# Performance work log

Hardware: AMD Instinct MI355X
Metric: run time of the kernel (lower is better)

The kernel has to match this reference:

```python
import jax, jax.numpy as jnp
import numpy as np

B, S, D, E, K = 2, 4096, 1024, 8, 2

def setup_inputs() -> dict:
    key = jax.random.key(0)
    k1, k2, k3, k4, k5 = jax.random.split(key, 5)
    x = jax.random.normal(k1, (B, S, D), dtype=jnp.float32)
    expert_weights = jax.random.uniform(k2, (B, S, K), dtype=jnp.float32)
    top_k_indices = jax.random.randint(k3, (B, S, K), 0, E, dtype=jnp.int32)
    W = jax.random.normal(k4, (E, D, D), dtype=jnp.float32) * (1.0 / np.sqrt(D))
    b = jax.random.normal(k5, (E, D), dtype=jnp.float32) * 0.01
    return {"x": x, "expert_weights": expert_weights,
            "top_k_indices": top_k_indices, "W": W, "b": b}

def reference(x, expert_weights, top_k_indices, W, b):
    # Dense all-expert linear: [B,S,E,Dout]
    expert_outputs = jnp.einsum('bsd,edf->bsef', x, W) + b  # bias broadcasts over b,s
    # Gather the top-k expert outputs per token: [B,S,K,Dout]
    gathered = jnp.take_along_axis(expert_outputs, top_k_indices[:, :, :, None], axis=2)
    # Weighted combine over k
    output = jnp.sum(expert_weights[:, :, :, None] * gathered, axis=2)
    return output
```

## Files before the change

kernel.cpp:

```cpp
#include <hip/hip_runtime.h>
#include <hip/hip_bf16.h>
#include <cstdio>
#include <cstdint>

static constexpr int TOK = 8192;
static constexpr int DIM = 1024;
static constexpr int NEXP = 8;
static constexpr int NGRP = 16;

typedef unsigned short u16;
typedef unsigned int u32;

using floatx4 = __attribute__((ext_vector_type(4))) float;
using bf16x8  = __attribute__((ext_vector_type(8))) __bf16;


__device__ __forceinline__ u16 f2bf(float f) {
  union { float f; u32 u; } v; v.f = f;
  u32 r = v.u + 0x7fffu + ((v.u >> 16) & 1u);
  return (u16)(r >> 16);
}

__device__ __forceinline__ float bf2f(u16 b) {
  union { u32 u; float f; } v; v.u = (u32)b << 16;
  return v.f;
}

__device__ __forceinline__ void gload_lds16(const void* g, void* l) {
  __builtin_amdgcn_global_load_lds(
      (const __attribute__((address_space(1))) void*)g,
      (__attribute__((address_space(3))) void*)l,
      16, 0, 0);
}

__global__ __launch_bounds__(1024)
void prep_kernel(const int* __restrict__ idx, const float* __restrict__ ew,
                 int* __restrict__ meta, int* __restrict__ tileMap,
                 int* __restrict__ tokList, float* __restrict__ wList,
                 int* __restrict__ posOf) {
  __shared__ int cnt2[16][NGRP];
  __shared__ int cur2[16][NGRP];
  __shared__ int tot[NGRP], offS[NGRP], tbase[NGRP];
  const int tid = threadIdx.x;
  const int wid = tid >> 6;
  if (tid < 16 * NGRP) ((int*)cnt2)[tid] = 0;
  __syncthreads();
  int gl[16];
#pragma unroll
  for (int j = 0; j < 16; ++j) {
    int i = tid + 1024 * j;
    int g = ((i & 1) << 3) | idx[i];
    gl[j] = g;
    atomicAdd(&cnt2[wid][g], 1);
  }
  __syncthreads();
  if (tid < NGRP) {
    int s = 0;
    for (int w = 0; w < 16; ++w) { cur2[w][tid] = s; s += cnt2[w][tid]; }
    tot[tid] = s;
  }
  __syncthreads();
  if (tid == 0) {
    int run = 0, t = 0, tk0 = 0;
    for (int g = 0; g < NGRP; ++g) {
      offS[g] = run; tbase[g] = t;
      t += (tot[g] + 127) >> 7;
      if (g == NEXP - 1) tk0 = t;
      run += tot[g];
    }
    meta[48] = t;
    meta[49] = tk0;
  }
  __syncthreads();
  if (tid < NGRP) {
    meta[tid] = tot[tid];
    meta[16 + tid] = offS[tid];
    int b = tbase[tid], n = (tot[tid] + 127) >> 7;
    for (int m0 = 0; m0 < n; ++m0) tileMap[b + m0] = (tid << 12) | m0;
  }
  if (tid < 16 * NGRP) {
    int w = tid >> 4, g = tid & 15;
    cur2[w][g] += offS[g];
  }
  __syncthreads();
#pragma unroll
  for (int j = 0; j < 16; ++j) {
    int i = tid + 1024 * j;
    int pos = atomicAdd(&cur2[wid][gl[j]], 1);
    tokList[pos] = i >> 1;
    wList[pos] = ew[i];
    posOf[i] = pos;
  }
}

__global__ __launch_bounds__(256)
void setup_kernel(const float* __restrict__ x, const int* __restrict__ posOf,
                  u16* __restrict__ Abuf, const float* __restrict__ W,
                  u16* __restrict__ wt) {
  const int bid = blockIdx.x;
  const int tid = threadIdx.x;
  if (bid < TOK) {
    const int t = bid;
    float4 v = reinterpret_cast<const float4*>(x + ((size_t)t << 10))[tid];
    ushort4 o;
    o.x = f2bf(v.x); o.y = f2bf(v.y); o.z = f2bf(v.z); o.w = f2bf(v.w);
    const int p0 = posOf[2 * t], p1 = posOf[2 * t + 1];
    reinterpret_cast<ushort4*>(Abuf + ((size_t)p0 << 10))[tid] = o;
    reinterpret_cast<ushort4*>(Abuf + ((size_t)p1 << 10))[tid] = o;
  } else {
    __shared__ u16 tile[32][33];
    const int b = bid - TOK;
    const int e = b >> 10;
    const int f0 = ((b >> 5) & 31) * 32, d0 = (b & 31) * 32;
    const float* src = W + ((size_t)e << 20);
    u16* dst = wt + ((size_t)e << 20);
    const int tx = tid & 31, ty = tid >> 5;
#pragma unroll
    for (int j = 0; j < 4; ++j) {
      int d = d0 + ty + 8 * j;
      tile[ty + 8 * j][tx] = f2bf(src[(size_t)d * DIM + f0 + tx]);
    }
    __syncthreads();
#pragma unroll
    for (int j = 0; j < 4; ++j) {
      int f = f0 + ty + 8 * j;
      dst[(size_t)f * DIM + d0 + tx] = tile[tx][ty + 8 * j];
    }
  }
}

__global__ __launch_bounds__(256, 4)
void moe_gemm_kernel(const u16* __restrict__ Abuf, const u16* __restrict__ wt,
                     const float* __restrict__ bias, const int* __restrict__ tokList,
                     const float* __restrict__ wList, const int* __restrict__ meta,
                     const int* __restrict__ tileMap, float* __restrict__ out,
                     u16* __restrict__ cbufA, u16* __restrict__ cbufB, int mode,
                     int pass) {
  constexpr int BM = 128, BN = 128, BK = 64;
  const int chunk = gridDim.y;
  int lin = blockIdx.y * 8 + blockIdx.x;
  int swz = (lin & 7) * chunk + (lin >> 3);
  int tileIdx = swz >> 3, nt = swz & 7;

  int tBase = 0, tEnd = meta[48];
  const int tilesK0 = meta[49];
  if (mode == 0) { if (pass == 0) tEnd = tilesK0; else tBase = tilesK0; }
  tileIdx += tBase;
  if (tileIdx >= tEnd) return;

  const int tm = tileMap[tileIdx];
  const int g = tm >> 12, m0 = tm & 0xfff;
  const int e = g & (NEXP - 1);
  const int nrem = meta[g] - m0 * BM;
  const int listBase = meta[16 + g] + m0 * BM;

  __shared__ __align__(16) u16 As[BM * BK];
  __shared__ __align__(16) u16 Bs[BN * BK];

  const int tid = threadIdx.x;
  const int rowA = tid >> 3;
  const int chnk = tid & 7;
  const int csw  = chnk ^ (rowA & 7);
  const u16* wb = wt + ((size_t)e << 20);
  const u16* ab = Abuf + ((size_t)listBase << 10);

  const int wid = tid >> 6, lane = tid & 63;
  const int wm = (wid >> 1) * 64, wn = (wid & 1) * 64;
  const int lr = lane & 15, lg = lane >> 4;
  const int rx = lr & 7;

  floatx4 acc[4][4];
#pragma unroll
  for (int i = 0; i < 4; ++i)
#pragma unroll
    for (int j = 0; j < 4; ++j) acc[i][j] = (floatx4){0.f, 0.f, 0.f, 0.f};

  for (int kt = 0; kt < DIM / BK; ++kt) {
    __syncthreads();
#pragma unroll
    for (int r = 0; r < 4; ++r) {
      const int row = rowA + 32 * r;
      gload_lds16(ab + ((size_t)row << 10) + kt * BK + csw * 8,
                  &As[row * BK + chnk * 8]);
    }
#pragma unroll
    for (int r = 0; r < 4; ++r) {
      const int row = rowA + 32 * r;
      gload_lds16(wb + ((size_t)(nt * BN + row) << 10) + kt * BK + csw * 8,
                  &Bs[row * BK + chnk * 8]);
    }
    asm volatile("s_waitcnt vmcnt(0)" ::: "memory");
    __syncthreads();

#pragma unroll
    for (int ks = 0; ks < 2; ++ks) {
      bf16x8 av[4], bv[4];
#pragma unroll
      for (int mi = 0; mi < 4; ++mi)
        av[mi] = *reinterpret_cast<const bf16x8*>(
            &As[(wm + mi * 16 + lr) * BK + (((ks * 4 + lg) ^ rx)) * 8]);
#pragma unroll
      for (int ni = 0; ni < 4; ++ni)
        bv[ni] = *reinterpret_cast<const bf16x8*>(
            &Bs[(wn + ni * 16 + lr) * BK + (((ks * 4 + lg) ^ rx)) * 8]);
#pragma unroll
      for (int mi = 0; mi < 4; ++mi)
#pragma unroll
        for (int ni = 0; ni < 4; ++ni)
          acc[mi][ni] = __builtin_amdgcn_mfma_f32_16x16x32_bf16(av[mi], bv[ni], acc[mi][ni], 0, 0, 0);
    }
  }

  u16* cb = nullptr;
  bool rmw = false, f32out = false;
  if (mode == 2)      cb = (g < NEXP) ? cbufA : cbufB;
  else if (mode == 1) { if (g < NEXP) f32out = true; else cb = cbufA; }
  else                { f32out = true; rmw = (pass == 1); }
  const float* bp = bias + e * DIM;
#pragma unroll
  for (int mi = 0; mi < 4; ++mi) {
#pragma unroll
    for (int r = 0; r < 4; ++r) {
      const int rl = wm + mi * 16 + lg * 4 + r;
      if (rl < nrem) {
        const int   tok = tokList[listBase + rl];
        const float w   = wList[listBase + rl];
        const size_t rowOff = (size_t)tok << 10;
#pragma unroll
        for (int ni = 0; ni < 4; ++ni) {
          const int col = nt * BN + wn + ni * 16 + lr;
          const float v = w * (acc[mi][ni][r] + bp[col]);
          if (f32out) { if (rmw) out[rowOff + col] += v; else out[rowOff + col] = v; }
          else        cb[rowOff + col] = f2bf(v);
        }
      }
    }
  }
}

__global__ __launch_bounds__(256)
void combine2_kernel(float* __restrict__ out, const u16* __restrict__ cbufA,
                     const u16* __restrict__ cbufB) {
  const int p = blockIdx.x * 256 + threadIdx.x;
  uint4 ca = reinterpret_cast<const uint4*>(cbufA)[p];
  uint4 cb = reinterpret_cast<const uint4*>(cbufB)[p];
  float4 r0, r1;
  r0.x = bf2f((u16)(ca.x & 0xffff)) + bf2f((u16)(cb.x & 0xffff));
  r0.y = bf2f((u16)(ca.x >> 16))    + bf2f((u16)(cb.x >> 16));
  r0.z = bf2f((u16)(ca.y & 0xffff)) + bf2f((u16)(cb.y & 0xffff));
  r0.w = bf2f((u16)(ca.y >> 16))    + bf2f((u16)(cb.y >> 16));
  r1.x = bf2f((u16)(ca.z & 0xffff)) + bf2f((u16)(cb.z & 0xffff));
  r1.y = bf2f((u16)(ca.z >> 16))    + bf2f((u16)(cb.z >> 16));
  r1.z = bf2f((u16)(ca.w & 0xffff)) + bf2f((u16)(cb.w & 0xffff));
  r1.w = bf2f((u16)(ca.w >> 16))    + bf2f((u16)(cb.w >> 16));
  float4* o4 = reinterpret_cast<float4*>(out) + 2 * (size_t)p;
  o4[0] = r0; o4[1] = r1;
}

__global__ __launch_bounds__(256)
void combine_kernel(float* __restrict__ out, const u16* __restrict__ cbuf) {
  const int p = blockIdx.x * 256 + threadIdx.x;
  uint4 c = reinterpret_cast<const uint4*>(cbuf)[p];
  float4* o4 = reinterpret_cast<float4*>(out) + 2 * (size_t)p;
  float4 a = o4[0], b = o4[1];
  a.x += bf2f((u16)(c.x & 0xffff)); a.y += bf2f((u16)(c.x >> 16));
  a.z += bf2f((u16)(c.y & 0xffff)); a.w += bf2f((u16)(c.y >> 16));
  b.x += bf2f((u16)(c.z & 0xffff)); b.y += bf2f((u16)(c.z >> 16));
  b.z += bf2f((u16)(c.w & 0xffff)); b.w += bf2f((u16)(c.w >> 16));
  o4[0] = a; o4[1] = b;
}

extern "C" void kernel_launch(void* const* d_in, const int* in_sizes, int n_in,
                              void* d_out, int out_size, void* d_ws, size_t ws_size,
                              hipStream_t stream) {
  const float* x    = (const float*)d_in[0];
  const float* ew   = (const float*)d_in[1];
  const int*   idx  = (const int*)d_in[2];
  const float* W    = (const float*)d_in[3];
  const float* bias = (const float*)d_in[4];
  float* out = (float*)d_out;

  char* ws = (char*)d_ws;
  u16*   Abuf  = (u16*)ws;
  u16*   wtp   = (u16*)(ws + ((size_t)32 << 20));
  u16*   cbufA = (u16*)(ws + ((size_t)48 << 20));
  u16*   cbufB = (u16*)(ws + ((size_t)64 << 20));

  const size_t tailSz = (size_t)(194 << 10);
  const size_t need0 = ((size_t)48 << 20) + tailSz;
  const size_t need1 = ((size_t)64 << 20) + tailSz;
  const size_t need2 = ((size_t)80 << 20) + tailSz;
  if (ws_size < need0) {
    fprintf(stderr, "kernel_launch: ws_size %zu < needed %zu\n", ws_size, need0);
    return;
  }
  const int mode = (ws_size >= need2) ? 2 : (ws_size >= need1) ? 1 : 0;
  char* tail = ws + ((mode == 2) ? ((size_t)80 << 20)
                                 : (mode == 1) ? ((size_t)64 << 20)
                                               : ((size_t)48 << 20));
  int*   tokList = (int*)tail;
  float* wList   = (float*)(tail + (64 << 10));
  int*   posOf   = (int*)(tail + (128 << 10));
  int*   meta    = (int*)(tail + (192 << 10));
  int*   tileMap = (int*)(tail + (193 << 10));

  prep_kernel<<<1, 1024, 0, stream>>>(idx, ew, meta, tileMap, tokList, wList, posOf);
  setup_kernel<<<TOK + 8192, 256, 0, stream>>>(x, posOf, Abuf, W, wtp);

  if (mode == 2) {
    moe_gemm_kernel<<<dim3(8, 144), 256, 0, stream>>>(
        Abuf, wtp, bias, tokList, wList, meta, tileMap, out, cbufA, cbufB, 2, 0);
    combine2_kernel<<<TOK * DIM / 8 / 256, 256, 0, stream>>>(out, cbufA, cbufB);
  } else if (mode == 1) {
    moe_gemm_kernel<<<dim3(8, 144), 256, 0, stream>>>(
        Abuf, wtp, bias, tokList, wList, meta, tileMap, out, cbufA, nullptr, 1, 0);
    combine_kernel<<<TOK * DIM / 8 / 256, 256, 0, stream>>>(out, cbufA);
  } else {
    moe_gemm_kernel<<<dim3(8, 72), 256, 0, stream>>>(
        Abuf, wtp, bias, tokList, wList, meta, tileMap, out, nullptr, nullptr, 0, 0);
    moe_gemm_kernel<<<dim3(8, 72), 256, 0, stream>>>(
        Abuf, wtp, bias, tokList, wList, meta, tileMap, out, nullptr, nullptr, 0, 1);
  }
}
```

Baseline: 116.5 us.

## Overlap routing prep with weight transpose and split x gather kernel

The single-block routing prep kernel now runs as an extra block inside the weight transpose/bf16 conversion launch, so it overlaps the weight work instead of running serially before it. The x gather/convert, which depends on posOf, moves into its own kernel launched afterwards. This takes the serial prep latency off the critical path. In exchange there is one extra launch, and the prep block now uses 256 threads doing 64 iterations each, so it runs longer on a single CU and could become the tail of the combined kernel.

```diff
diff --git a/kernel.cpp b/kernel.cpp
--- a/kernel.cpp
+++ b/kernel.cpp
@@ -33,85 +33,18 @@
       16, 0, 0);
 }
 
-__global__ __launch_bounds__(1024)
-void prep_kernel(const int* __restrict__ idx, const float* __restrict__ ew,
-                 int* __restrict__ meta, int* __restrict__ tileMap,
-                 int* __restrict__ tokList, float* __restrict__ wList,
-                 int* __restrict__ posOf) {
-  __shared__ int cnt2[16][NGRP];
-  __shared__ int cur2[16][NGRP];
-  __shared__ int tot[NGRP], offS[NGRP], tbase[NGRP];
-  const int tid = threadIdx.x;
-  const int wid = tid >> 6;
-  if (tid < 16 * NGRP) ((int*)cnt2)[tid] = 0;
-  __syncthreads();
-  int gl[16];
-#pragma unroll
-  for (int j = 0; j < 16; ++j) {
-    int i = tid + 1024 * j;
-    int g = ((i & 1) << 3) | idx[i];
-    gl[j] = g;
-    atomicAdd(&cnt2[wid][g], 1);
-  }
-  __syncthreads();
-  if (tid < NGRP) {
-    int s = 0;
-    for (int w = 0; w < 16; ++w) { cur2[w][tid] = s; s += cnt2[w][tid]; }
-    tot[tid] = s;
-  }
-  __syncthreads();
-  if (tid == 0) {
-    int run = 0, t = 0, tk0 = 0;
-    for (int g = 0; g < NGRP; ++g) {
-      offS[g] = run; tbase[g] = t;
-      t += (tot[g] + 127) >> 7;
-      if (g == NEXP - 1) tk0 = t;
-      run += tot[g];
-    }
-    meta[48] = t;
-    meta[49] = tk0;
-  }
-  __syncthreads();
-  if (tid < NGRP) {
-    meta[tid] = tot[tid];
-    meta[16 + tid] = offS[tid];
-    int b = tbase[tid], n = (tot[tid] + 127) >> 7;
-    for (int m0 = 0; m0 < n; ++m0) tileMap[b + m0] = (tid << 12) | m0;
-  }
-  if (tid < 16 * NGRP) {
-    int w = tid >> 4, g = tid & 15;
-    cur2[w][g] += offS[g];
-  }
-  __syncthreads();
-#pragma unroll
-  for (int j = 0; j < 16; ++j) {
-    int i = tid + 1024 * j;
-    int pos = atomicAdd(&cur2[wid][gl[j]], 1);
-    tokList[pos] = i >> 1;
-    wList[pos] = ew[i];
-    posOf[i] = pos;
-  }
-}
-
 __global__ __launch_bounds__(256)
-void setup_kernel(const float* __restrict__ x, const int* __restrict__ posOf,
-                  u16* __restrict__ Abuf, const float* __restrict__ W,
-                  u16* __restrict__ wt) {
+void trans_prep_kernel(const float* __restrict__ W, u16* __restrict__ wt,
+                       const int* __restrict__ idx, const float* __restrict__ ew,
+                       int* __restrict__ meta, int* __restrict__ tileMap,
+                       int* __restrict__ tokList, float* __restrict__ wList,
+                       int* __restrict__ posOf) {
   const int bid = blockIdx.x;
   const int tid = threadIdx.x;
-  if (bid < TOK) {
-    const int t = bid;
-    float4 v = reinterpret_cast<const float4*>(x + ((size_t)t << 10))[tid];
-    ushort4 o;
-    o.x = f2bf(v.x); o.y = f2bf(v.y); o.z = f2bf(v.z); o.w = f2bf(v.w);
-    const int p0 = posOf[2 * t], p1 = posOf[2 * t + 1];
-    reinterpret_cast<ushort4*>(Abuf + ((size_t)p0 << 10))[tid] = o;
-    reinterpret_cast<ushort4*>(Abuf + ((size_t)p1 << 10))[tid] = o;
-  } else {
+  if (bid < 8192) {
     __shared__ u16 tile[32][33];
-    const int b = bid - TOK;
-    const int e = b >> 10;
-    const int f0 = ((b >> 5) & 31) * 32, d0 = (b & 31) * 32;
+    const int e = bid >> 10;
+    const int f0 = ((bid >> 5) & 31) * 32, d0 = (bid & 31) * 32;
     const float* src = W + ((size_t)e << 20);
     u16* dst = wt + ((size_t)e << 20);
     const int tx = tid & 31, ty = tid >> 5;
@@ -126,7 +59,69 @@
       int f = f0 + ty + 8 * j;
       dst[(size_t)f * DIM + d0 + tx] = tile[tx][ty + 8 * j];
     }
-  }
+  } else {
+    __shared__ int cnt2[4][NGRP];
+    __shared__ int cur2[4][NGRP];
+    __shared__ int tot[NGRP], offS[NGRP], tbase[NGRP];
+    const int wid = tid >> 6;
+    if (tid < 4 * NGRP) ((int*)cnt2)[tid] = 0;
+    __syncthreads();
+    for (int j = 0; j < 64; ++j) {
+      int i = tid + 256 * j;
+      int g = ((i & 1) << 3) | idx[i];
+      atomicAdd(&cnt2[wid][g], 1);
+    }
+    __syncthreads();
+    if (tid < NGRP) {
+      int s = 0;
+      for (int w = 0; w < 4; ++w) { cur2[w][tid] = s; s += cnt2[w][tid]; }
+      tot[tid] = s;
+    }
+    __syncthreads();
+    if (tid == 0) {
+      int run = 0, t = 0, tk0 = 0;
+      for (int g = 0; g < NGRP; ++g) {
+        offS[g] = run; tbase[g] = t;
+        t += (tot[g] + 127) >> 7;
+        if (g == NEXP - 1) tk0 = t;
+        run += tot[g];
+      }
+      meta[48] = t;
+      meta[49] = tk0;
+    }
+    __syncthreads();
+    if (tid < NGRP) {
+      meta[tid] = tot[tid];
+      meta[16 + tid] = offS[tid];
+      int b = tbase[tid], n = (tot[tid] + 127) >> 7;
+      for (int m0 = 0; m0 < n; ++m0) tileMap[b + m0] = (tid << 12) | m0;
+    }
+    if (tid < 4 * NGRP) {
+      int w = tid >> 4, g = tid & 15;
+      cur2[w][g] += offS[g];
+    }
+    __syncthreads();
+    for (int j = 0; j < 64; ++j) {
+      int i = tid + 256 * j;
+      int g = ((i & 1) << 3) | idx[i];
+      int pos = atomicAdd(&cur2[wid][g], 1);
+      tokList[pos] = i >> 1;
+      wList[pos] = ew[i];
+      posOf[i] = pos;
+    }
+  }
+}
+
+__global__ __launch_bounds__(256)
+void gather_x_kernel(const float* __restrict__ x, const int* __restrict__ posOf,
+                     u16* __restrict__ Abuf) {
+  const int t = blockIdx.x, tid = threadIdx.x;
+  float4 v = reinterpret_cast<const float4*>(x + ((size_t)t << 10))[tid];
+  ushort4 o;
+  o.x = f2bf(v.x); o.y = f2bf(v.y); o.z = f2bf(v.z); o.w = f2bf(v.w);
+  const int p0 = posOf[2 * t], p1 = posOf[2 * t + 1];
+  reinterpret_cast<ushort4*>(Abuf + ((size_t)p0 << 10))[tid] = o;
+  reinterpret_cast<ushort4*>(Abuf + ((size_t)p1 << 10))[tid] = o;
 }
 
 __global__ __launch_bounds__(256, 4)
@@ -304,8 +299,9 @@
   int*   meta    = (int*)(tail + (192 << 10));
   int*   tileMap = (int*)(tail + (193 << 10));
 
-  prep_kernel<<<1, 1024, 0, stream>>>(idx, ew, meta, tileMap, tokList, wList, posOf);
-  setup_kernel<<<TOK + 8192, 256, 0, stream>>>(x, posOf, Abuf, W, wtp);
+  trans_prep_kernel<<<8193, 256, 0, stream>>>(W, wtp, idx, ew, meta, tileMap,
+                                              tokList, wList, posOf);
+  gather_x_kernel<<<TOK, 256, 0, stream>>>(x, posOf, Abuf);
 
   if (mode == 2) {
     moe_gemm_kernel<<<dim3(8, 144), 256, 0, stream>>>(
```

New measurement: 133.1 us. 14.2% more time.

## Overlap routing prep with weight transpose in one fused kernel launch

Applied to the files above, without the earlier changes.

The single-block routing/prefix-sum prep kernel is merged into the W transpose/bf16 conversion kernel as an extra block, so the serial routing work runs alongside the transpose instead of before it. Each 1024-thread transpose block now handles four 32x32 tiles. The token gather/convert is split out into its own kernel launched afterwards, since it depends on posOf. This removes the idle time of a one-block launch, at the cost of one more launch and a larger block with a shared __syncthreads across the four sub-tiles.

```diff
diff --git a/kernel.cpp b/kernel.cpp
--- a/kernel.cpp
+++ b/kernel.cpp
@@ -34,99 +34,100 @@
 }
 
 __global__ __launch_bounds__(1024)
-void prep_kernel(const int* __restrict__ idx, const float* __restrict__ ew,
-                 int* __restrict__ meta, int* __restrict__ tileMap,
-                 int* __restrict__ tokList, float* __restrict__ wList,
-                 int* __restrict__ posOf) {
-  __shared__ int cnt2[16][NGRP];
-  __shared__ int cur2[16][NGRP];
-  __shared__ int tot[NGRP], offS[NGRP], tbase[NGRP];
-  const int tid = threadIdx.x;
-  const int wid = tid >> 6;
-  if (tid < 16 * NGRP) ((int*)cnt2)[tid] = 0;
-  __syncthreads();
-  int gl[16];
-#pragma unroll
-  for (int j = 0; j < 16; ++j) {
-    int i = tid + 1024 * j;
-    int g = ((i & 1) << 3) | idx[i];
-    gl[j] = g;
-    atomicAdd(&cnt2[wid][g], 1);
-  }
-  __syncthreads();
-  if (tid < NGRP) {
-    int s = 0;
-    for (int w = 0; w < 16; ++w) { cur2[w][tid] = s; s += cnt2[w][tid]; }
-    tot[tid] = s;
-  }
-  __syncthreads();
-  if (tid == 0) {
-    int run = 0, t = 0, tk0 = 0;
-    for (int g = 0; g < NGRP; ++g) {
-      offS[g] = run; tbase[g] = t;
-      t += (tot[g] + 127) >> 7;
-      if (g == NEXP - 1) tk0 = t;
-      run += tot[g];
-    }
-    meta[48] = t;
-    meta[49] = tk0;
-  }
-  __syncthreads();
-  if (tid < NGRP) {
-    meta[tid] = tot[tid];
-    meta[16 + tid] = offS[tid];
-    int b = tbase[tid], n = (tot[tid] + 127) >> 7;
-    for (int m0 = 0; m0 < n; ++m0) tileMap[b + m0] = (tid << 12) | m0;
-  }
-  if (tid < 16 * NGRP) {
-    int w = tid >> 4, g = tid & 15;
-    cur2[w][g] += offS[g];
-  }
-  __syncthreads();
-#pragma unroll
-  for (int j = 0; j < 16; ++j) {
-    int i = tid + 1024 * j;
-    int pos = atomicAdd(&cur2[wid][gl[j]], 1);
-    tokList[pos] = i >> 1;
-    wList[pos] = ew[i];
-    posOf[i] = pos;
-  }
-}
-
-__global__ __launch_bounds__(256)
-void setup_kernel(const float* __restrict__ x, const int* __restrict__ posOf,
-                  u16* __restrict__ Abuf, const float* __restrict__ W,
-                  u16* __restrict__ wt) {
+void trans_prep_kernel(const float* __restrict__ W, u16* __restrict__ wt,
+                       const int* __restrict__ idx, const float* __restrict__ ew,
+                       int* __restrict__ meta, int* __restrict__ tileMap,
+                       int* __restrict__ tokList, float* __restrict__ wList,
+                       int* __restrict__ posOf) {
   const int bid = blockIdx.x;
   const int tid = threadIdx.x;
-  if (bid < TOK) {
-    const int t = bid;
-    float4 v = reinterpret_cast<const float4*>(x + ((size_t)t << 10))[tid];
-    ushort4 o;
-    o.x = f2bf(v.x); o.y = f2bf(v.y); o.z = f2bf(v.z); o.w = f2bf(v.w);
-    const int p0 = posOf[2 * t], p1 = posOf[2 * t + 1];
-    reinterpret_cast<ushort4*>(Abuf + ((size_t)p0 << 10))[tid] = o;
-    reinterpret_cast<ushort4*>(Abuf + ((size_t)p1 << 10))[tid] = o;
-  } else {
-    __shared__ u16 tile[32][33];
-    const int b = bid - TOK;
-    const int e = b >> 10;
-    const int f0 = ((b >> 5) & 31) * 32, d0 = (b & 31) * 32;
+  if (bid < 2048) {
+    __shared__ u16 tile4[4][32][33];
+    const int sub = tid >> 8;
+    const int t4 = bid * 4 + sub;
+    const int e = t4 >> 10;
+    const int f0 = ((t4 >> 5) & 31) * 32, d0 = (t4 & 31) * 32;
     const float* src = W + ((size_t)e << 20);
     u16* dst = wt + ((size_t)e << 20);
-    const int tx = tid & 31, ty = tid >> 5;
+    const int tl = tid & 255;
+    const int tx = tl & 31, ty = tl >> 5;
 #pragma unroll
     for (int j = 0; j < 4; ++j) {
       int d = d0 + ty + 8 * j;
-      tile[ty + 8 * j][tx] = f2bf(src[(size_t)d * DIM + f0 + tx]);
+      tile4[sub][ty + 8 * j][tx] = f2bf(src[(size_t)d * DIM + f0 + tx]);
     }
     __syncthreads();
 #pragma unroll
     for (int j = 0; j < 4; ++j) {
       int f = f0 + ty + 8 * j;
-      dst[(size_t)f * DIM + d0 + tx] = tile[tx][ty + 8 * j];
-    }
-  }
+      dst[(size_t)f * DIM + d0 + tx] = tile4[sub][tx][ty + 8 * j];
+    }
+  } else {
+    __shared__ int cnt2[16][NGRP];
+    __shared__ int cur2[16][NGRP];
+    __shared__ int tot[NGRP], offS[NGRP], tbase[NGRP];
+    const int wid = tid >> 6;
+    if (tid < 16 * NGRP) ((int*)cnt2)[tid] = 0;
+    __syncthreads();
+    int gl[16];
+#pragma unroll
+    for (int j = 0; j < 16; ++j) {
+      int i = tid + 1024 * j;
+      int g = ((i & 1) << 3) | idx[i];
+      gl[j] = g;
+      atomicAdd(&cnt2[wid][g], 1);
+    }
+    __syncthreads();
+    if (tid < NGRP) {
+      int s = 0;
+      for (int w = 0; w < 16; ++w) { cur2[w][tid] = s; s += cnt2[w][tid]; }
+      tot[tid] = s;
+    }
+    __syncthreads();
+    if (tid == 0) {
+      int run = 0, t = 0, tk0 = 0;
+      for (int g = 0; g < NGRP; ++g) {
+        offS[g] = run; tbase[g] = t;
+        t += (tot[g] + 127) >> 7;
+        if (g == NEXP - 1) tk0 = t;
+        run += tot[g];
+      }
+      meta[48] = t;
+      meta[49] = tk0;
+    }
+    __syncthreads();
+    if (tid < NGRP) {
+      meta[tid] = tot[tid];
+      meta[16 + tid] = offS[tid];
+      int b = tbase[tid], n = (tot[tid] + 127) >> 7;
+      for (int m0 = 0; m0 < n; ++m0) tileMap[b + m0] = (tid << 12) | m0;
+    }
+    if (tid < 16 * NGRP) {
+      int w = tid >> 4, g = tid & 15;
+      cur2[w][g] += offS[g];
+    }
+    __syncthreads();
+#pragma unroll
+    for (int j = 0; j < 16; ++j) {
+      int i = tid + 1024 * j;
+      int pos = atomicAdd(&cur2[wid][gl[j]], 1);
+      tokList[pos] = i >> 1;
+      wList[pos] = ew[i];
+      posOf[i] = pos;
+    }
+  }
+}
+
+__global__ __launch_bounds__(256)
+void gather_x_kernel(const float* __restrict__ x, const int* __restrict__ posOf,
+                     u16* __restrict__ Abuf) {
+  const int t = blockIdx.x, tid = threadIdx.x;
+  float4 v = reinterpret_cast<const float4*>(x + ((size_t)t << 10))[tid];
+  ushort4 o;
+  o.x = f2bf(v.x); o.y = f2bf(v.y); o.z = f2bf(v.z); o.w = f2bf(v.w);
+  const int p0 = posOf[2 * t], p1 = posOf[2 * t + 1];
+  reinterpret_cast<ushort4*>(Abuf + ((size_t)p0 << 10))[tid] = o;
+  reinterpret_cast<ushort4*>(Abuf + ((size_t)p1 << 10))[tid] = o;
 }
 
 __global__ __launch_bounds__(256, 4)
@@ -304,8 +305,9 @@
   int*   meta    = (int*)(tail + (192 << 10));
   int*   tileMap = (int*)(tail + (193 << 10));
 
-  prep_kernel<<<1, 1024, 0, stream>>>(idx, ew, meta, tileMap, tokList, wList, posOf);
-  setup_kernel<<<TOK + 8192, 256, 0, stream>>>(x, posOf, Abuf, W, wtp);
+  trans_prep_kernel<<<2049, 1024, 0, stream>>>(W, wtp, idx, ew, meta, tileMap,
+                                               tokList, wList, posOf);
+  gather_x_kernel<<<TOK, 256, 0, stream>>>(x, posOf, Abuf);
 
   if (mode == 2) {
     moe_gemm_kernel<<<dim3(8, 144), 256, 0, stream>>>(
```

Result: no change. 116.8 us (median of 2 runs) (+0.3%).
